# Optimization experiments

Hardware: AMD Instinct MI355X
Metric: run time of the kernel (lower is better)

The kernel has to match this reference:

```python
import jax, jax.numpy as jnp
import numpy as np

TAU = 0.2  # world.kgc_temp
EPS = 1e-12  # F.normalize eps


def _l2_normalize(z):
    n = jnp.linalg.norm(z, axis=1, keepdims=True)
    return z / jnp.maximum(n, EPS)


def setup_inputs() -> dict:
    key = jax.random.key(0)
    k1, k2 = jax.random.split(key)
    N, D = 8192, 512
    z1 = jax.random.normal(k1, (N, D), dtype=jnp.float32)
    z2 = jax.random.normal(k2, (N, D), dtype=jnp.float32)
    return {"z1": z1, "z2": z2}


def _semi_loss(h1, h2):
    # h1, h2: [N, D] already L2-normalized
    refl_sim = jnp.exp(jnp.matmul(h1, h1.T) / TAU)      # [N, N]
    between_sim = jnp.exp(jnp.matmul(h1, h2.T) / TAU)   # [N, N]
    denom = refl_sim.sum(axis=1) + between_sim.sum(axis=1) - jnp.diag(refl_sim)
    return -jnp.log(jnp.diag(between_sim) / denom)      # [N]


def reference(z1, z2):
    h1 = _l2_normalize(z1)
    h2 = _l2_normalize(z2)
    l1 = _semi_loss(h1, h2)
    l2 = _semi_loss(h2, h1)
    return jnp.sum((l1 + l2) * 0.5)
```

## Files before the change

### kernel.cpp

```cpp
#include <hip/hip_runtime.h>
#include <hip/hip_bf16.h>
#include <math.h>
#include <stdint.h>

#define N_ROWS 8192
#define DIM 512
#define INV_TAU 5.0f
#define EXP5 148.41315910257660342f

typedef float f32x4 __attribute__((ext_vector_type(4)));
typedef int   i32x4 __attribute__((ext_vector_type(4)));
typedef int   i32x8 __attribute__((ext_vector_type(8)));

union Frag8 {
  i32x8 v8;
  struct { i32x4 lo, hi; } s;
};

__device__ __forceinline__ void gload_lds16(const void* g, void* l) {
  __builtin_amdgcn_global_load_lds(
      (__attribute__((address_space(1))) void*)(void*)g,
      (__attribute__((address_space(3))) void*)l,
      16, 0, 0);
}

__global__ __launch_bounds__(256) void normalize_kernel(
    const float* __restrict__ z1, const float* __restrict__ z2,
    uint8_t* __restrict__ h1p, uint8_t* __restrict__ h2p,
    float* __restrict__ dvec,
    float* __restrict__ r1, float* __restrict__ r2,
    float* __restrict__ brow, float* __restrict__ bcol,
    float* __restrict__ out) {
  __shared__ __align__(16) uint8_t L[16384];
  const int t = threadIdx.x;
  const int lr = t >> 4;
  const int kb = t & 15;
  const int row = blockIdx.x * 16 + lr;
  const float4* p1 = (const float4*)(z1 + (size_t)row * DIM + kb * 32);
  const float4* p2 = (const float4*)(z2 + (size_t)row * DIM + kb * 32);
  float4 a[8], b[8];
  float s1 = 0.f, s2 = 0.f, s3 = 0.f;
#pragma unroll
  for (int i = 0; i < 8; i++) {
    a[i] = p1[i]; b[i] = p2[i];
    s1 += a[i].x*a[i].x + a[i].y*a[i].y + a[i].z*a[i].z + a[i].w*a[i].w;
    s2 += b[i].x*b[i].x + b[i].y*b[i].y + b[i].z*b[i].z + b[i].w*b[i].w;
    s3 += a[i].x*b[i].x + a[i].y*b[i].y + a[i].z*b[i].z + a[i].w*b[i].w;
  }
  for (int m = 1; m <= 8; m <<= 1) {
    s1 += __shfl_xor(s1, m);
    s2 += __shfl_xor(s2, m);
    s3 += __shfl_xor(s3, m);
  }
  const float inv1 = 1.0f / fmaxf(sqrtf(s1), 1e-12f);
  const float inv2 = 1.0f / fmaxf(sqrtf(s2), 1e-12f);
  int w1[8], w2[8];
#pragma unroll
  for (int i = 0; i < 8; i++) {
    int w = __builtin_amdgcn_cvt_pk_fp8_f32(a[i].x*inv1, a[i].y*inv1, 0, false);
    w1[i] = __builtin_amdgcn_cvt_pk_fp8_f32(a[i].z*inv1, a[i].w*inv1, w, true);
    w = __builtin_amdgcn_cvt_pk_fp8_f32(b[i].x*inv2, b[i].y*inv2, 0, false);
    w2[i] = __builtin_amdgcn_cvt_pk_fp8_f32(b[i].z*inv2, b[i].w*inv2, w, true);
  }
  const int ks = kb >> 2;
  const int l = (kb & 3) * 16 + lr;
  *(int4*)(L + ks * 2048 + l * 16)          = make_int4(w1[0], w1[1], w1[2], w1[3]);
  *(int4*)(L + ks * 2048 + 1024 + l * 16)   = make_int4(w1[4], w1[5], w1[6], w1[7]);
  *(int4*)(L + 8192 + ks * 2048 + l * 16)        = make_int4(w2[0], w2[1], w2[2], w2[3]);
  *(int4*)(L + 8192 + ks * 2048 + 1024 + l * 16) = make_int4(w2[4], w2[5], w2[6], w2[7]);
  if (kb == 0) dvec[row] = s3 * inv1 * inv2;
  if (t < 16) {
    const int i = blockIdx.x * 16 + t;
    r1[i] = 0.f; r2[i] = 0.f; brow[i] = 0.f; bcol[i] = 0.f;
    if (i == 0) out[0] = 0.f;
  }
  __syncthreads();
  const size_t gb = (size_t)blockIdx.x * 8192;
  int4* g1 = (int4*)(h1p + gb);
  int4* g2 = (int4*)(h2p + gb);
  const int4* Lv = (const int4*)L;
  g1[t]       = Lv[t];
  g1[t + 256] = Lv[t + 256];
  g2[t]       = Lv[t + 512];
  g2[t + 256] = Lv[t + 768];
}

__global__ __launch_bounds__(256) void expsum_kernel(
    const uint8_t* __restrict__ h1p, const uint8_t* __restrict__ h2p,
    float* __restrict__ r1, float* __restrict__ r2,
    float* __restrict__ brow, float* __restrict__ bcol) {
  __shared__ __align__(16) uint8_t Bs[65536];

  const int u = (blockIdx.x & 7) * 1032 + (blockIdx.x >> 3);
  int bj = (int)((sqrt(8.0 * (double)u + 1.0) - 1.0) * 0.5);
  if (bj * (bj + 1) / 2 > u) bj--;
  if ((bj + 1) * (bj + 2) / 2 <= u) bj++;
  const int bi = u - bj * (bj + 1) / 2;
  const bool diagb = (bi == bj);

  const uint8_t* Ap = (bi < 64) ? h1p : h2p;
  const uint8_t* Bp = (bj < 64) ? h1p : h2p;
  float* rowsOut = (bi < 64) ? ((bj < 64) ? r1 : brow) : r2;
  float* colsOut = (bj < 64) ? r1 : ((bi < 64) ? bcol : r2);
  const int iOutBase = (bi & 63) * 128;
  const int jOutBase = (bj & 63) * 128;

  const int t = threadIdx.x;
  const int w = t >> 6;
  const int lane = t & 63;
  const int l16 = lane & 15;
  const int kq = lane >> 4;

  const uint8_t* Ag =
      Ap + ((size_t)((bi & 63) * 8 + w * 2)) * 8192 + (size_t)lane * 16 + 4096;
  Frag8 Af[2][4];
#pragma unroll
  for (int f = 0; f < 2; f++)
#pragma unroll
    for (int ks = 0; ks < 4; ks++) {
      const int ofs = f * 8192 + ks * 2048 - 4096;
      Af[f][ks].s.lo = *(const i32x4*)(Ag + ofs);
      Af[f][ks].s.hi = *(const i32x4*)(Ag + ofs + 1024);
    }

  {
    const uint8_t* Bgp = Bp + (size_t)(bj & 63) * 65536;
#pragma unroll
    for (int rnd = 0; rnd < 16; rnd++)
      gload_lds16(Bgp + rnd * 4096 + t * 16, Bs + rnd * 4096 + t * 16);
  }

  f32x4 acc[2][8];
#pragma unroll
  for (int a = 0; a < 2; a++)
#pragma unroll
    for (int b = 0; b < 8; b++)
#pragma unroll
      for (int r = 0; r < 4; r++) acc[a][b][r] = 0.0f;

  const uint8_t* BsL = Bs + lane * 16;

  __syncthreads();

#pragma unroll
  for (int ks = 0; ks < 4; ks++) {
    Frag8 Bf[8];
#pragma unroll
    for (int fn = 0; fn < 8; fn++) {
      Bf[fn].s.lo = *(const i32x4*)(BsL + fn * 8192 + ks * 2048);
      Bf[fn].s.hi = *(const i32x4*)(BsL + fn * 8192 + ks * 2048 + 1024);
    }
#pragma unroll
    for (int fm = 0; fm < 2; fm++)
#pragma unroll
      for (int fn = 0; fn < 8; fn++)
        acc[fm][fn] = __builtin_amdgcn_mfma_scale_f32_16x16x128_f8f6f4(
            Af[fm][ks].v8, Bf[fn].v8, acc[fm][fn],
            0, 0,
            0, 0x7F7F7F7F,
            0, 0x7F7F7F7F);
  }

  float rowp[2][4];
  float colp[8];
#pragma unroll
  for (int fm = 0; fm < 2; fm++)
#pragma unroll
    for (int r = 0; r < 4; r++) rowp[fm][r] = 0.0f;
#pragma unroll
  for (int fn = 0; fn < 8; fn++) colp[fn] = 0.0f;

  if (!diagb) {
#pragma unroll
    for (int fm = 0; fm < 2; fm++)
#pragma unroll
      for (int fn = 0; fn < 8; fn++)
#pragma unroll
        for (int r = 0; r < 4; r++) {
          const float e = __expf(acc[fm][fn][r] * INV_TAU);
          rowp[fm][r] += e;
          colp[fn] += e;
        }
  } else {
#pragma unroll
    for (int fm = 0; fm < 2; fm++)
#pragma unroll
      for (int fn = 0; fn < 8; fn++)
#pragma unroll
        for (int r = 0; r < 4; r++) {
          const int ti = w * 32 + fm * 16 + kq * 4 + r;
          const int tj = fn * 16 + l16;
          const float e = __expf(acc[fm][fn][r] * INV_TAU);
          rowp[fm][r] += (ti <= tj) ? e : 0.0f;
          colp[fn] += (ti < tj) ? e : 0.0f;
        }
  }

  __syncthreads();
  float* lds_col = (float*)Bs;
  float* lds_row = lds_col + 128;
  if (t < 128) lds_col[t] = 0.0f;
  __syncthreads();

#pragma unroll
  for (int fm = 0; fm < 2; fm++) {
#pragma unroll
    for (int r = 0; r < 4; r++) {
      float v = rowp[fm][r];
      v += __shfl_xor(v, 1);
      v += __shfl_xor(v, 2);
      v += __shfl_xor(v, 4);
      v += __shfl_xor(v, 8);
      if (l16 == 0) lds_row[w * 32 + fm * 16 + kq * 4 + r] = v;
    }
  }
#pragma unroll
  for (int fn = 0; fn < 8; fn++) {
    float v = colp[fn];
    v += __shfl_xor(v, 16);
    v += __shfl_xor(v, 32);
    if (kq == 0) atomicAdd(&lds_col[fn * 16 + l16], v);
  }
  __syncthreads();

  if (t < 128) atomicAdd(&rowsOut[iOutBase + t], lds_row[t]);
  else         atomicAdd(&colsOut[jOutBase + (t - 128)], lds_col[t - 128]);
}

__global__ __launch_bounds__(256) void finalize_kernel(
    const float* __restrict__ r1, const float* __restrict__ r2,
    const float* __restrict__ brow, const float* __restrict__ bcol,
    const float* __restrict__ dvec, float* __restrict__ out) {
  const int i = blockIdx.x * 256 + threadIdx.x;
  const float den1 = r1[i] + brow[i] - EXP5;
  const float den2 = r2[i] + bcol[i] - EXP5;
  float v = 0.5f * (logf(den1) + logf(den2)) - INV_TAU * dvec[i];
  for (int m = 32; m; m >>= 1) v += __shfl_xor(v, m);
  __shared__ float red[4];
  const int wave = threadIdx.x >> 6;
  if ((threadIdx.x & 63) == 0) red[wave] = v;
  __syncthreads();
  if (threadIdx.x == 0) atomicAdd(out, red[0] + red[1] + red[2] + red[3]);
}

extern "C" void kernel_launch(void* const* d_in, const int* in_sizes, int n_in,
                              void* d_out, int out_size, void* d_ws, size_t ws_size,
                              hipStream_t stream) {
  const float* z1 = (const float*)d_in[0];
  const float* z2 = (const float*)d_in[1];
  float* out = (float*)d_out;

  char* ws = (char*)d_ws;
  uint8_t* h1p = (uint8_t*)ws;
  uint8_t* h2p = (uint8_t*)(ws + (4u << 20));
  float* r1   = (float*)(ws + (8u << 20));
  float* r2   = r1 + N_ROWS;
  float* brow = r2 + N_ROWS;
  float* bcol = brow + N_ROWS;
  float* dvec = bcol + N_ROWS;

  normalize_kernel<<<N_ROWS / 16, 256, 0, stream>>>(
      z1, z2, h1p, h2p, dvec, r1, r2, brow, bcol, out);
  expsum_kernel<<<8256, 256, 0, stream>>>(h1p, h2p, r1, r2, brow, bcol);
  finalize_kernel<<<N_ROWS / 256, 256, 0, stream>>>(r1, r2, brow, bcol, dvec, out);
}
```

Measured before the change: 200.6 us.

## Double-buffer B tile in LDS by K-chunk to overlap loads with MFMA

Measured after the change: 182.5 us. 9.0% less time.

```diff
diff --git a/kernel.cpp b/kernel.cpp
--- a/kernel.cpp
+++ b/kernel.cpp
@@ -85,11 +85,11 @@
   g2[t + 256] = Lv[t + 768];
 }
 
-__global__ __launch_bounds__(256) void expsum_kernel(
+__global__ __launch_bounds__(256, 3) void expsum_kernel(
     const uint8_t* __restrict__ h1p, const uint8_t* __restrict__ h2p,
     float* __restrict__ r1, float* __restrict__ r2,
     float* __restrict__ brow, float* __restrict__ bcol) {
-  __shared__ __align__(16) uint8_t Bs[65536];
+  __shared__ __align__(16) uint8_t Bs[32768];
 
   const int u = (blockIdx.x & 7) * 1032 + (blockIdx.x >> 3);
   int bj = (int)((sqrt(8.0 * (double)u + 1.0) - 1.0) * 0.5);
@@ -122,13 +122,43 @@
       Af[f][ks].s.lo = *(const i32x4*)(Ag + ofs);
       Af[f][ks].s.hi = *(const i32x4*)(Ag + ofs + 1024);
     }
-
-  {
-    const uint8_t* Bgp = Bp + (size_t)(bj & 63) * 65536;
-#pragma unroll
-    for (int rnd = 0; rnd < 16; rnd++)
-      gload_lds16(Bgp + rnd * 4096 + t * 16, Bs + rnd * 4096 + t * 16);
-  }
+  __builtin_amdgcn_sched_barrier(0);
+
+  const uint8_t* Bgp = Bp + (size_t)(bj & 63) * 65536;
+
+#define STAGE(KS, BUFOFS)                                                   \
+  do {                                                                      \
+    _Pragma("unroll") for (int r_ = 0; r_ < 4; r_++) {                      \
+      const int cb_ = (r_ * 256 + t) * 16;                                  \
+      gload_lds16(Bgp + ((cb_ >> 11) << 13) + (KS)*2048 + (cb_ & 2047),     \
+                  Bs + (BUFOFS) + cb_);                                     \
+    }                                                                       \
+  } while (0)
+
+#define COMPUTE_CHUNK(KS, BUFOFS)                                           \
+  do {                                                                      \
+    const uint8_t* Bc_ = (const uint8_t*)Bs + (BUFOFS) + lane * 16;         \
+    _Pragma("unroll") for (int fp_ = 0; fp_ < 4; fp_++) {                   \
+      Frag8 B0_, B1_;                                                       \
+      B0_.s.lo = *(const i32x4*)(Bc_ + (2 * fp_ + 0) * 2048);               \
+      B0_.s.hi = *(const i32x4*)(Bc_ + (2 * fp_ + 0) * 2048 + 1024);        \
+      B1_.s.lo = *(const i32x4*)(Bc_ + (2 * fp_ + 1) * 2048);               \
+      B1_.s.hi = *(const i32x4*)(Bc_ + (2 * fp_ + 1) * 2048 + 1024);        \
+      _Pragma("unroll") for (int fm_ = 0; fm_ < 2; fm_++) {                 \
+        acc[fm_][2 * fp_ + 0] =                                             \
+            __builtin_amdgcn_mfma_scale_f32_16x16x128_f8f6f4(               \
+                Af[fm_][KS].v8, B0_.v8, acc[fm_][2 * fp_ + 0],              \
+                0, 0, 0, 0x7F7F7F7F, 0, 0x7F7F7F7F);                        \
+        acc[fm_][2 * fp_ + 1] =                                             \
+            __builtin_amdgcn_mfma_scale_f32_16x16x128_f8f6f4(               \
+                Af[fm_][KS].v8, B1_.v8, acc[fm_][2 * fp_ + 1],              \
+                0, 0, 0, 0x7F7F7F7F, 0, 0x7F7F7F7F);                        \
+      }                                                                     \
+    }                                                                       \
+  } while (0)
+
+  STAGE(0, 0);
+  STAGE(1, 16384);
 
   f32x4 acc[2][8];
 #pragma unroll
@@ -138,28 +168,34 @@
 #pragma unroll
       for (int r = 0; r < 4; r++) acc[a][b][r] = 0.0f;
 
-  const uint8_t* BsL = Bs + lane * 16;
-
-  __syncthreads();
-
-#pragma unroll
-  for (int ks = 0; ks < 4; ks++) {
-    Frag8 Bf[8];
-#pragma unroll
-    for (int fn = 0; fn < 8; fn++) {
-      Bf[fn].s.lo = *(const i32x4*)(BsL + fn * 8192 + ks * 2048);
-      Bf[fn].s.hi = *(const i32x4*)(BsL + fn * 8192 + ks * 2048 + 1024);
-    }
-#pragma unroll
-    for (int fm = 0; fm < 2; fm++)
-#pragma unroll
-      for (int fn = 0; fn < 8; fn++)
-        acc[fm][fn] = __builtin_amdgcn_mfma_scale_f32_16x16x128_f8f6f4(
-            Af[fm][ks].v8, Bf[fn].v8, acc[fm][fn],
-            0, 0,
-            0, 0x7F7F7F7F,
-            0, 0x7F7F7F7F);
-  }
+  asm volatile("s_waitcnt vmcnt(4)" ::: "memory");
+  __builtin_amdgcn_s_barrier();
+  __builtin_amdgcn_sched_barrier(0);
+  COMPUTE_CHUNK(0, 0);
+  __builtin_amdgcn_sched_barrier(0);
+  __builtin_amdgcn_s_barrier();
+  STAGE(2, 0);
+
+  asm volatile("s_waitcnt vmcnt(4)" ::: "memory");
+  __builtin_amdgcn_s_barrier();
+  __builtin_amdgcn_sched_barrier(0);
+  COMPUTE_CHUNK(1, 16384);
+  __builtin_amdgcn_sched_barrier(0);
+  __builtin_amdgcn_s_barrier();
+  STAGE(3, 16384);
+
+  asm volatile("s_waitcnt vmcnt(4)" ::: "memory");
+  __builtin_amdgcn_s_barrier();
+  __builtin_amdgcn_sched_barrier(0);
+  COMPUTE_CHUNK(2, 0);
+
+  asm volatile("s_waitcnt vmcnt(0)" ::: "memory");
+  __builtin_amdgcn_s_barrier();
+  __builtin_amdgcn_sched_barrier(0);
+  COMPUTE_CHUNK(3, 16384);
+
+#undef STAGE
+#undef COMPUTE_CHUNK
 
   float rowp[2][4];
   float colp[8];
```
